# Optimization experiments

Hardware: AMD Instinct MI355X
Metric: run time of the kernel (lower is better)

The kernel has to match this reference:

```python
import jax, jax.numpy as jnp
import numpy as np

EPS = 1e-10

def setup_inputs() -> dict:
    key = jax.random.key(0)
    ks = jax.random.split(key, 7)
    B, S, C, H, W = 8, 4, 512, 64, 64
    Cq = C // 4
    x = jax.random.normal(ks[0], (B, S, C, H, W), dtype=jnp.float32)
    wq = jax.random.normal(ks[1], (S, Cq, C), dtype=jnp.float32) * 0.02
    bq = jax.random.normal(ks[2], (S, Cq), dtype=jnp.float32) * 0.02
    wk = jax.random.normal(ks[3], (S, Cq, C), dtype=jnp.float32) * 0.02
    bk = jax.random.normal(ks[4], (S, Cq), dtype=jnp.float32) * 0.02
    wv = jax.random.normal(ks[5], (S, C, C), dtype=jnp.float32) * 0.02
    bv = jax.random.normal(ks[6], (S, C), dtype=jnp.float32) * 0.02
    gamma = jnp.zeros((1,), dtype=jnp.float32)
    return {"x": x, "wq": wq, "bq": bq, "wk": wk, "bk": bk,
            "wv": wv, "bv": bv, "gamma": gamma}

def reference(x, wq, bq, wk, bk, wv, bv, gamma):
    # x: (B, S, C, H, W); per-scale 1x1 convs == per-pixel matmuls
    B, S, C, H, W = x.shape
    q = jnp.einsum('bschw,soc->bsohw', x, wq) + bq[None, :, :, None, None]
    k = jnp.einsum('bschw,soc->bsohw', x, wk) + bk[None, :, :, None, None]
    v = jnp.einsum('bschw,soc->bsohw', x, wv) + bv[None, :, :, None, None]
    pq = q.reshape(B, S, -1)                      # (B, S, D)
    pk = k.reshape(B, S, -1).transpose(0, 2, 1)   # (B, D, S)
    pv = v.reshape(B, S, -1)                      # (B, S, C*H*W)
    # L2 normalization (cosine similarity), matching torch eps placement
    A1 = pq / (jnp.sqrt(jnp.sum(pq * pq, axis=-1, keepdims=True)) + EPS)
    B1 = pk / (jnp.sqrt(jnp.sum(pk * pk, axis=1, keepdims=True)) + EPS)
    energy = jnp.einsum('bsd,bdt->bst', A1, B1)   # (B, S, S)
    attention = jax.nn.softmax(energy, axis=-1)
    out = jnp.einsum('bst,btd->bsd', attention, pv).reshape(B, S, C, H, W)
    out = gamma[0] * out + x
    # original returns list [out[:, i]] for i in range(S); return stacked tensor
    return out
```

## Files before the change

kernel.cpp:

```cpp
#include <hip/hip_runtime.h>
#include <hip/hip_bf16.h>

#define EPS_F 1e-10f

typedef short s16x8 __attribute__((ext_vector_type(8)));
typedef float f32x4 __attribute__((ext_vector_type(4)));
typedef unsigned short ushort_t;

constexpr int B_ = 8, S_ = 4, C_ = 512, Cq_ = 128, HW_ = 4096;
constexpr long long D_ = (long long)Cq_ * HW_;

__device__ inline float bf_lo(unsigned int u) { return __uint_as_float(u << 16); }
__device__ inline float bf_hi(unsigned int u) { return __uint_as_float(u & 0xffff0000u); }

__device__ inline ushort_t f2bf(float f) {
    __hip_bfloat16 h = __float2bfloat16(f);
    return *reinterpret_cast<ushort_t*>(&h);
}
__device__ inline unsigned int pack_bf2(float a, float b) {
    return (unsigned int)f2bf(a) | ((unsigned int)f2bf(b) << 16);
}
__device__ inline float dot8(uint4 a, uint4 b) {
    return bf_lo(a.x) * bf_lo(b.x) + bf_hi(a.x) * bf_hi(b.x)
         + bf_lo(a.y) * bf_lo(b.y) + bf_hi(a.y) * bf_hi(b.y)
         + bf_lo(a.z) * bf_lo(b.z) + bf_hi(a.z) * bf_hi(b.z)
         + bf_lo(a.w) * bf_lo(b.w) + bf_hi(a.w) * bf_hi(b.w);
}

#define GLOAD16(gp, lp) __builtin_amdgcn_global_load_lds( \
    (const __attribute__((address_space(1))) unsigned int*)(gp), \
    (__attribute__((address_space(3))) unsigned int*)(lp), 16, 0, 0)

#define VMCNT(n) asm volatile("s_waitcnt vmcnt(" #n ")" ::: "memory")
#define LGK0     asm volatile("s_waitcnt lgkmcnt(0)" ::: "memory")
#define MFMA16(a, b, c) __builtin_amdgcn_mfma_f32_16x16x32_bf16(a, b, c, 0, 0, 0)

__global__ __launch_bounds__(256) void prep3(
    const float* __restrict__ wq, const float* __restrict__ wk,
    const float* __restrict__ wv,
    ushort_t* __restrict__ Wqk_pre, ushort_t* __restrict__ Wvb_pre,
    float* __restrict__ g4) {
    int gid = blockIdx.x * 256 + threadIdx.x;
    if (gid < 8 * 24 * 16) g4[gid] = 0.f;
    if (gid < 65536) {
        int s = gid >> 14;
        int kt = (gid >> 11) & 7;
        int row = (gid >> 3) & 255;
        int slot = gid & 7;
        int col = kt * 64 + ((slot ^ (row & 7)) << 3);
        const float* src = (row < 128)
            ? &wq[((size_t)s * 128 + row) * 512 + col]
            : &wk[((size_t)s * 128 + (row - 128)) * 512 + col];
        float4 f0 = *reinterpret_cast<const float4*>(src);
        float4 f1 = *reinterpret_cast<const float4*>(src + 4);
        uint4 o;
        o.x = pack_bf2(f0.x, f0.y); o.y = pack_bf2(f0.z, f0.w);
        o.z = pack_bf2(f1.x, f1.y); o.w = pack_bf2(f1.z, f1.w);
        *reinterpret_cast<uint4*>(Wqk_pre + (size_t)gid * 8) = o;
    } else {
        int c2 = gid - 65536;
        int t = c2 >> 15;
        int ct = (c2 >> 14) & 1;
        int kt = (c2 >> 11) & 7;
        int row = (c2 >> 3) & 255;
        int slot = c2 & 7;
        int col = kt * 64 + ((slot ^ (row & 7)) << 3);
        const float* src = &wv[((size_t)t * 512 + ct * 256 + row) * 512 + col];
        float4 f0 = *reinterpret_cast<const float4*>(src);
        float4 f1 = *reinterpret_cast<const float4*>(src + 4);
        uint4 o;
        o.x = pack_bf2(f0.x, f0.y); o.y = pack_bf2(f0.z, f0.w);
        o.z = pack_bf2(f1.x, f1.y); o.w = pack_bf2(f1.z, f1.w);
        *reinterpret_cast<uint4*>(Wvb_pre + (size_t)c2 * 8) = o;
    }
}

#define STAGE_A(T, bufidx)                                                   \
    { const ushort_t* _tp = ASRC(T);                                         \
      ushort_t* _ld = &AsAll[(bufidx) * 16384];                              \
      _Pragma("unroll")                                                      \
      for (int _i = 0; _i < 4; ++_i)                                         \
          GLOAD16(_tp + ((w4 + _i) << 9) + (lane << 3),                      \
                  _ld + ((w4 + _i) << 9)); }

#define LOAD_B(T, V0, V1)                                                    \
    { const float* _s = BSRC(T);                                             \
      V0 = *reinterpret_cast<const float4*>(_s);                             \
      V1 = *reinterpret_cast<const float4*>(_s + 4); }

#define WRITE_B(bufidx, V0, V1)                                              \
    { float _vv[8] = {V0.x, V0.y, V0.z, V0.w, V1.x, V1.y, V1.z, V1.w};       \
      ushort_t* _bd = &BsAll[(bufidx) * 4096 + bw_row0];                     \
      _Pragma("unroll")                                                      \
      for (int _j = 0; _j < 8; ++_j)                                         \
          _bd[_j * 64 + ((bw_sb ^ _j) << 3)] = f2bf(_vv[_j]); }

#define COMPUTE(bufidx)                                                      \
    { const int _ab = (bufidx) * 16384, _bb = (bufidx) * 4096;               \
      _Pragma("unroll")                                                      \
      for (int h = 0; h < 2; ++h) {                                          \
          s16x8 af0 = *reinterpret_cast<const s16x8*>(                       \
              &AsAll[_ab + (arow + 0 * 16 + li) * 64 + a_sl[h]]);            \
          s16x8 af1 = *reinterpret_cast<const s16x8*>(                       \
              &AsAll[_ab + (arow + 1 * 16 + li) * 64 + a_sl[h]]);            \
          s16x8 af2 = *reinterpret_cast<const s16x8*>(                       \
              &AsAll[_ab + (arow + 2 * 16 + li) * 64 + a_sl[h]]);            \
          s16x8 af3 = *reinterpret_cast<const s16x8*>(                       \
              &AsAll[_ab + (arow + 3 * 16 + li) * 64 + a_sl[h]]);            \
          s16x8 bf0 = *reinterpret_cast<const s16x8*>(                       \
              &BsAll[_bb + bp0 * 64 + b_sl0[h]]);                            \
          s16x8 bf1 = *reinterpret_cast<const s16x8*>(                       \
              &BsAll[_bb + bp1 * 64 + b_sl1[h]]);                            \
          __builtin_amdgcn_s_setprio(1);                                     \
          acc[0][0] = MFMA16(af0, bf0, acc[0][0]);                           \
          acc[0][1] = MFMA16(af0, bf1, acc[0][1]);                           \
          acc[1][0] = MFMA16(af1, bf0, acc[1][0]);                           \
          acc[1][1] = MFMA16(af1, bf1, acc[1][1]);                           \
          acc[2][0] = MFMA16(af2, bf0, acc[2][0]);                           \
          acc[2][1] = MFMA16(af2, bf1, acc[2][1]);                           \
          acc[3][0] = MFMA16(af3, bf0, acc[3][0]);                           \
          acc[3][1] = MFMA16(af3, bf1, acc[3][1]);                           \
          __builtin_amdgcn_s_setprio(0);                                     \
      } }

#define PIPE_PROLOGUE()                                                      \
    LOAD_B(0, nbE0, nbE1);                                                   \
    STAGE_A(0, 0);                                                           \
    LOAD_B(1, nbO0, nbO1);                                                   \
    STAGE_A(1, 1);                                                           \
    VMCNT(10);                                                               \
    WRITE_B(0, nbE0, nbE1);                                                  \
    VMCNT(6);                                                                \
    LGK0;                                                                    \
    __builtin_amdgcn_s_barrier();

#define PIPE_ITER(T, WB0, WB1, LB0, LB1)                                     \
    {                                                                        \
        const int _t = (T);                                                  \
        if (_t + 1 < NT) { VMCNT(4); WRITE_B(oN, WB0, WB1); }                \
        if (_t + 2 < NT) { LOAD_B(_t + 2, LB0, LB1); STAGE_A(_t + 2, oNN); } \
        COMPUTE(oC);                                                         \
        ITER_EXTRA(_t);                                                      \
        if (_t + 1 < NT) {                                                   \
            if (_t + 2 < NT) { VMCNT(6); } else { VMCNT(0); }                \
            LGK0;                                                            \
            __builtin_amdgcn_s_barrier();                                    \
        }                                                                    \
        int _r = oC; oC = oN; oN = oNN; oNN = _r;                            \
    }

#define PIPE_COMMON_DECLS()                                                  \
    const int tid = threadIdx.x;                                             \
    const int w = tid >> 6, lane = tid & 63;                                 \
    const int w4 = w * 4;                                                    \
    const int wr = w >> 1, wc = w & 1;                                       \
    const int li = lane & 15, lk = lane >> 4;                                \
    const int arow = wr * 64;                                                \
    const int bp0 = wc * 32 + li, bp1 = wc * 32 + 16 + li;                   \
    int a_sl[2], b_sl0[2], b_sl1[2];                                         \
    _Pragma("unroll")                                                        \
    for (int h = 0; h < 2; ++h) {                                            \
        a_sl[h] = (((h * 4 + lk) ^ (li & 7)) << 3);                          \
        b_sl0[h] = (((h * 4 + lk) ^ ((bp0 >> 3) & 7) ^ (bp0 & 7)) << 3);     \
        b_sl1[h] = (((h * 4 + lk) ^ ((bp1 >> 3) & 7) ^ (bp1 & 7)) << 3);     \
    }                                                                        \
    const int sk = tid >> 3, sp = (tid & 7) * 8;                             \
    const int bw_row0 = sp * 64 + ((tid >> 3) & 7);                          \
    const int bw_sb = (tid >> 6) ^ (tid & 7);                                \
    int oC = 0, oN = 1, oNN = 2;                                             \
    float4 nbE0, nbE1, nbO0, nbO1;                                           \
    f32x4 acc[4][2];                                                         \
    _Pragma("unroll")                                                        \
    for (int mf = 0; mf < 4; ++mf)                                           \
        _Pragma("unroll")                                                    \
        for (int nf = 0; nf < 2; ++nf) acc[mf][nf] = 0.f;

#define ASRC(T) (Wqk_pre + ((size_t)(s * 8 + (T)) << 14))
#define BSRC(T) (x + (size_t)bt * C_ * HW_ + (size_t)((T) * 64 + sk) * HW_ + p0 + sp)
#define ITER_EXTRA(T)

__global__ __launch_bounds__(512) void qk4(
    const ushort_t* __restrict__ Wqk_pre, const float* __restrict__ x,
    const float* __restrict__ bq, const float* __restrict__ bk,
    ushort_t* __restrict__ Qb, ushort_t* __restrict__ Kb) {

    constexpr int NT = 8;
    const int id = ((blockIdx.x & 7) << 8) | (blockIdx.x >> 3);
    const int bt = id >> 6;
    const int s = bt & 3;
    const int p0 = (id & 63) * 64;

    __shared__ __align__(16) ushort_t AsAll[3 * 16384];
    __shared__ __align__(16) ushort_t BsAll[3 * 4096];

    PIPE_COMMON_DECLS();
    PIPE_PROLOGUE();

    for (int t0 = 0; t0 < NT; t0 += 2) {
        PIPE_ITER(t0,     nbO0, nbO1, nbE0, nbE1);
        PIPE_ITER(t0 + 1, nbE0, nbE1, nbO0, nbO1);
    }

#pragma unroll
    for (int mf = 0; mf < 4; ++mf) {
#pragma unroll
        for (int r = 0; r < 4; ++r) {
            int m = wr * 64 + mf * 16 + lk * 4 + r;
            float bias = (m < 128) ? bq[s * 128 + m] : bk[s * 128 + (m - 128)];
#pragma unroll
            for (int nf = 0; nf < 2; ++nf) {
                int p = p0 + wc * 32 + nf * 16 + li;
                float vv = acc[mf][nf][r] + bias;
                if (m < 128)
                    Qb[(size_t)bt * D_ + (size_t)m * HW_ + p] = f2bf(vv);
                else
                    Kb[(size_t)bt * D_ + (size_t)(m - 128) * HW_ + p] = f2bf(vv);
            }
        }
    }
}
#undef ASRC
#undef BSRC
#undef ITER_EXTRA

#define ASRC(T) (Wvb_pre + (((size_t)(((T) >> 3) * 2 + ct) * 8 + ((T) & 7)) << 14))
#define BSRC(T) (x + ((size_t)(b * 4 + ((T) >> 3)) * 512 + ((T) & 7) * 64 + sk) * HW_ + p0 + sp)
#define ITER_EXTRA(T)                                                        \
    if (((T) & 7) == 7) {                                                    \
        const int _t2 = (T) >> 3;                                            \
        float _wv[4];                                                        \
        _Pragma("unroll")                                                    \
        for (int _so = 0; _so < 4; ++_so) _wv[_so] = attL[_so * 4 + _t2];    \
        _Pragma("unroll")                                                    \
        for (int _so = 0; _so < 4; ++_so)                                    \
            _Pragma("unroll")                                                \
            for (int _mf = 0; _mf < 4; ++_mf)                                \
                _Pragma("unroll")                                            \
                for (int _nf = 0; _nf < 2; ++_nf)                            \
                    mst[_so][_mf][_nf] += _wv[_so] * acc[_mf][_nf];          \
        _Pragma("unroll")                                                    \
        for (int _mf = 0; _mf < 4; ++_mf)                                    \
            _Pragma("unroll")                                                \
            for (int _nf = 0; _nf < 2; ++_nf) acc[_mf][_nf] = 0.f;           \
    }

__global__ __launch_bounds__(512) void vblend4(
    const ushort_t* __restrict__ Wvb_pre, const float* __restrict__ x,
    const float* __restrict__ bv, const float* __restrict__ att,
    const float* __restrict__ gamma, float* __restrict__ out) {

    constexpr int NT = 32;
    const int id = ((blockIdx.x & 7) << 7) | (blockIdx.x >> 3);
    const int b = id >> 7;
    const int ct = (id >> 6) & 1;
    const int p0 = (id & 63) * 64;

    __shared__ __align__(16) ushort_t AsAll[3 * 16384];
    __shared__ __align__(16) ushort_t BsAll[3 * 4096];
    __shared__ float attL[16];

    if (threadIdx.x < 16) attL[threadIdx.x] = att[b * 16 + threadIdx.x];
    __syncthreads();

    PIPE_COMMON_DECLS();

    f32x4 mst[4][4][2];
#pragma unroll
    for (int so = 0; so < 4; ++so)
#pragma unroll
        for (int mf = 0; mf < 4; ++mf)
#pragma unroll
            for (int nf = 0; nf < 2; ++nf) mst[so][mf][nf] = 0.f;

    PIPE_PROLOGUE();

    for (int t0 = 0; t0 < NT; t0 += 2) {
        PIPE_ITER(t0,     nbO0, nbO1, nbE0, nbE1);
        PIPE_ITER(t0 + 1, nbE0, nbE1, nbO0, nbO1);
    }

    const float gm = gamma[0];
    const int c0 = ct * 256;
#pragma unroll
    for (int mf = 0; mf < 4; ++mf) {
#pragma unroll
        for (int r = 0; r < 4; ++r) {
            int c = c0 + wr * 64 + mf * 16 + lk * 4 + r;
            float bvv[4];
#pragma unroll
            for (int t = 0; t < 4; ++t) bvv[t] = bv[(size_t)t * 512 + c];
#pragma unroll
            for (int so = 0; so < 4; ++so) {
                float bsum = attL[so * 4 + 0] * bvv[0] + attL[so * 4 + 1] * bvv[1]
                           + attL[so * 4 + 2] * bvv[2] + attL[so * 4 + 3] * bvv[3];
#pragma unroll
                for (int nf = 0; nf < 2; ++nf) {
                    int p = p0 + wc * 32 + nf * 16 + li;
                    size_t off = ((size_t)(b * 4 + so) * C_ + c) * HW_ + p;
                    out[off] = gm * (mst[so][mf][nf][r] + bsum) + x[off];
                }
            }
        }
    }
}
#undef ASRC
#undef BSRC
#undef ITER_EXTRA

__global__ __launch_bounds__(256) void gram5(
    const ushort_t* __restrict__ Q, const ushort_t* __restrict__ K,
    float* __restrict__ g4) {

    const int ch = blockIdx.x;
    const int b  = blockIdx.y;
    const size_t base = (size_t)ch * (D_ / 16);

    const uint4* qv[4];
    const uint4* kv[4];
#pragma unroll
    for (int s = 0; s < 4; ++s) {
        qv[s] = reinterpret_cast<const uint4*>(Q + (size_t)(b * 4 + s) * D_ + base);
        kv[s] = reinterpret_cast<const uint4*>(K + (size_t)(b * 4 + s) * D_ + base);
    }

    float accr[24];
#pragma unroll
    for (int e = 0; e < 24; ++e) accr[e] = 0.f;

    const int n8 = (int)(D_ / 16 / 8);
    for (int i = threadIdx.x; i < n8; i += 256) {
        uint4 qa[4], ka[4];
#pragma unroll
        for (int s = 0; s < 4; ++s) { qa[s] = qv[s][i]; ka[s] = kv[s][i]; }
#pragma unroll
        for (int s = 0; s < 4; ++s) {
#pragma unroll
            for (int u = 0; u < 4; ++u) accr[s * 4 + u] += dot8(qa[s], ka[u]);
            accr[16 + s] += dot8(qa[s], qa[s]);
            accr[20 + s] += dot8(ka[s], ka[s]);
        }
    }

    __shared__ float red[4][24];
    const int lane = threadIdx.x & 63, wid = threadIdx.x >> 6;
#pragma unroll
    for (int e = 0; e < 24; ++e) {
        float v = accr[e];
#pragma unroll
        for (int o = 32; o > 0; o >>= 1) v += __shfl_down(v, o);
        if (lane == 0) red[wid][e] = v;
    }
    __syncthreads();
    if (threadIdx.x < 24) {
        float t = red[0][threadIdx.x] + red[1][threadIdx.x]
                + red[2][threadIdx.x] + red[3][threadIdx.x];
        g4[((size_t)b * 24 + threadIdx.x) * 16 + ch] = t;
    }
}

__global__ void att_k5(const float* __restrict__ g4, float* __restrict__ att) {
    const int b = threadIdx.x;
    if (b >= B_) return;
    float e_[24];
#pragma unroll
    for (int e = 0; e < 24; ++e) {
        const float* p = g4 + ((size_t)b * 24 + e) * 16;
        float t = 0.f;
#pragma unroll
        for (int ch = 0; ch < 16; ++ch) t += p[ch];
        e_[e] = t;
    }
    float nq[4], nk[4];
#pragma unroll
    for (int s = 0; s < 4; ++s) {
        nq[s] = sqrtf(e_[16 + s]) + EPS_F;
        nk[s] = sqrtf(e_[20 + s]) + EPS_F;
    }
#pragma unroll
    for (int s = 0; s < 4; ++s) {
        float e[4], m = -1e30f;
#pragma unroll
        for (int t = 0; t < 4; ++t) {
            e[t] = e_[s * 4 + t] / (nq[s] * nk[t]);
            m = fmaxf(m, e[t]);
        }
        float sum = 0.f;
#pragma unroll
        for (int t = 0; t < 4; ++t) { e[t] = expf(e[t] - m); sum += e[t]; }
#pragma unroll
        for (int t = 0; t < 4; ++t) att[(size_t)(b * 4 + s) * 4 + t] = e[t] / sum;
    }
}

extern "C" void kernel_launch(void* const* d_in, const int* in_sizes, int n_in,
                              void* d_out, int out_size, void* d_ws, size_t ws_size,
                              hipStream_t stream) {
    const float* x     = (const float*)d_in[0];
    const float* wq    = (const float*)d_in[1];
    const float* bq    = (const float*)d_in[2];
    const float* wk    = (const float*)d_in[3];
    const float* bk    = (const float*)d_in[4];
    const float* wv    = (const float*)d_in[5];
    const float* bv    = (const float*)d_in[6];
    const float* gamma = (const float*)d_in[7];
    float* out = (float*)d_out;

    char* ws = (char*)d_ws;
    const size_t qk_elems = (size_t)B_ * S_ * Cq_ * HW_;
    ushort_t* Qb      = (ushort_t*)ws;
    ushort_t* Kb      = Qb + qk_elems;
    ushort_t* Wqk_pre = Kb + qk_elems;
    ushort_t* Wvb_pre = Wqk_pre + (size_t)4 * 8 * 256 * 64;
    float*    g4      = (float*)(Wvb_pre + (size_t)4 * 2 * 8 * 256 * 64);
    float*    att     = g4 + 8 * 24 * 16;

    prep3<<<768, 256, 0, stream>>>(wq, wk, wv, Wqk_pre, Wvb_pre, g4);
    qk4<<<2048, 512, 0, stream>>>(Wqk_pre, x, bq, bk, Qb, Kb);
    gram5<<<dim3(16, 8), 256, 0, stream>>>(Qb, Kb, g4);
    att_k5<<<1, 64, 0, stream>>>(g4, att);
    vblend4<<<1024, 512, 0, stream>>>(Wvb_pre, x, bv, att, gamma, out);
}
```

Measured before the change: 429.7 us.

## Emit transposed bf16 copy of x in QK kernel and reuse it in V-blend

The QK projection kernel now writes the bf16, swizzled, pixel-major tile of x it already staged in LDS out to a workspace buffer. The V-blend kernel then loads this bf16 tile directly with 16-byte global-to-LDS loads instead of re-reading and converting fp32 x. This halves the bytes x contributes to the V pass and removes the conversion work there. In exchange the QK pass writes an extra 32 MB buffer and needs more workspace; if the workspace is too small it falls back to the old path.

```diff
diff --git a/kernel.cpp b/kernel.cpp
--- a/kernel.cpp
+++ b/kernel.cpp
@@ -219,6 +219,80 @@
         }
     }
 }
+
+__global__ __launch_bounds__(512) void qk5(
+    const ushort_t* __restrict__ Wqk_pre, const float* __restrict__ x,
+    const float* __restrict__ bq, const float* __restrict__ bk,
+    ushort_t* __restrict__ Qb, ushort_t* __restrict__ Kb,
+    ushort_t* __restrict__ xbfT) {
+
+    const int blk = blockIdx.x;
+    const int bt = (blk & 7) * 4 + ((blk >> 3) >> 6);
+    const int s = bt & 3;
+    const int p0 = ((blk >> 3) & 63) * 64;
+
+    __shared__ __align__(16) ushort_t AsAll[3 * 16384];
+    __shared__ __align__(16) ushort_t BsAll[3 * 4096];
+
+    PIPE_COMMON_DECLS();
+
+    const int ep = tid >> 3, esl = tid & 7;
+    const int ec = esl ^ ((ep >> 3) & 7) ^ (ep & 7);
+    ushort_t* emit_base = xbfT + ((size_t)bt * HW_ + p0 + ep) * 512 + ec * 8;
+
+    LOAD_B(0, nbE0, nbE1);
+    STAGE_A(0, 0);
+    LOAD_B(1, nbO0, nbO1);
+    STAGE_A(1, 1);
+    VMCNT(10);
+    WRITE_B(0, nbE0, nbE1);
+    VMCNT(6);
+    LGK0;
+    __builtin_amdgcn_s_barrier();
+
+#pragma unroll
+    for (int t = 0; t < 8; ++t) {
+        if (t + 1 < 8) {
+            if (t == 0) { VMCNT(4); } else { VMCNT(5); }
+            if ((t + 1) & 1) { WRITE_B((t + 1) % 3, nbO0, nbO1); }
+            else             { WRITE_B((t + 1) % 3, nbE0, nbE1); }
+        }
+        if (t + 2 < 8) {
+            if ((t + 2) & 1) { LOAD_B(t + 2, nbO0, nbO1); }
+            else             { LOAD_B(t + 2, nbE0, nbE1); }
+            STAGE_A(t + 2, (t + 2) % 3);
+        }
+        COMPUTE(t % 3);
+        {
+            s16x8 ev = *reinterpret_cast<const s16x8*>(
+                &BsAll[(t % 3) * 4096 + ep * 64 + esl * 8]);
+            *reinterpret_cast<s16x8*>(emit_base + t * 64) = ev;
+        }
+        if (t + 1 < 8) {
+            if (t + 2 < 8) { VMCNT(7); } else { VMCNT(1); }
+            LGK0;
+            __builtin_amdgcn_s_barrier();
+        }
+    }
+
+#pragma unroll
+    for (int mf = 0; mf < 4; ++mf) {
+#pragma unroll
+        for (int r = 0; r < 4; ++r) {
+            int m = wr * 64 + mf * 16 + lk * 4 + r;
+            float bias = (m < 128) ? bq[s * 128 + m] : bk[s * 128 + (m - 128)];
+#pragma unroll
+            for (int nf = 0; nf < 2; ++nf) {
+                int p = p0 + wc * 32 + nf * 16 + li;
+                float vv = acc[mf][nf][r] + bias;
+                if (m < 128)
+                    Qb[(size_t)bt * D_ + (size_t)m * HW_ + p] = f2bf(vv);
+                else
+                    Kb[(size_t)bt * D_ + (size_t)(m - 128) * HW_ + p] = f2bf(vv);
+            }
+        }
+    }
+}
 #undef ASRC
 #undef BSRC
 #undef ITER_EXTRA
@@ -307,6 +381,135 @@
 #undef BSRC
 #undef ITER_EXTRA
 
+__global__ __launch_bounds__(512) void vblend5(
+    const ushort_t* __restrict__ Wvb_pre, const ushort_t* __restrict__ xbfT,
+    const float* __restrict__ x, const float* __restrict__ bv,
+    const float* __restrict__ att, const float* __restrict__ gamma,
+    float* __restrict__ out) {
+
+    const int blk = blockIdx.x;
+    const int b = blk & 7;
+    const int r_ = blk >> 3;
+    const int ct = r_ >> 6;
+    const int p0 = (r_ & 63) * 64;
+
+    __shared__ __align__(16) ushort_t AsAll[3 * 16384];
+    __shared__ __align__(16) ushort_t BsAll[3 * 4096];
+    __shared__ float attL[16];
+
+    if (threadIdx.x < 16) attL[threadIdx.x] = att[b * 16 + threadIdx.x];
+    __syncthreads();
+
+    const int tid = threadIdx.x;
+    const int w = tid >> 6, lane = tid & 63;
+    const int w4 = w * 4;
+    const int wr = w >> 1, wc = w & 1;
+    const int li = lane & 15, lk = lane >> 4;
+    const int arow = wr * 64;
+    const int bp0 = wc * 32 + li, bp1 = wc * 32 + 16 + li;
+    int a_sl[2], b_sl0[2], b_sl1[2];
+#pragma unroll
+    for (int h = 0; h < 2; ++h) {
+        a_sl[h] = (((h * 4 + lk) ^ (li & 7)) << 3);
+        b_sl0[h] = (((h * 4 + lk) ^ ((bp0 >> 3) & 7) ^ (bp0 & 7)) << 3);
+        b_sl1[h] = (((h * 4 + lk) ^ ((bp1 >> 3) & 7) ^ (bp1 & 7)) << 3);
+    }
+    const int sp_ = tid >> 3;
+    const int sc_ = (tid & 7) ^ ((sp_ >> 3) & 7) ^ (sp_ & 7);
+    const ushort_t* bsrc_base = xbfT + ((size_t)b * 4 * HW_) * 512
+                                + ((size_t)(p0 + sp_)) * 512 + sc_ * 8;
+
+    f32x4 acc[4][2];
+#pragma unroll
+    for (int mf = 0; mf < 4; ++mf)
+#pragma unroll
+        for (int nf = 0; nf < 2; ++nf) acc[mf][nf] = 0.f;
+    f32x4 mst[4][4][2];
+#pragma unroll
+    for (int so = 0; so < 4; ++so)
+#pragma unroll
+        for (int mf = 0; mf < 4; ++mf)
+#pragma unroll
+            for (int nf = 0; nf < 2; ++nf) mst[so][mf][nf] = 0.f;
+
+#define STAGE5(T, BUF)                                                       \
+    {   const int _t5 = (T);                                                 \
+        const ushort_t* _ap = Wvb_pre +                                      \
+            (((size_t)((_t5 >> 3) * 2 + ct) * 8 + (_t5 & 7)) << 14);         \
+        ushort_t* _al = &AsAll[(BUF) * 16384];                               \
+        _Pragma("unroll")                                                    \
+        for (int _i = 0; _i < 4; ++_i)                                       \
+            GLOAD16(_ap + ((w4 + _i) << 9) + (lane << 3),                    \
+                    _al + ((w4 + _i) << 9));                                 \
+        const ushort_t* _bp = bsrc_base + (size_t)(_t5 >> 3) * HW_ * 512     \
+                              + (_t5 & 7) * 64;                              \
+        GLOAD16(_bp, &BsAll[(BUF) * 4096 + w * 512]);                        \
+    }
+
+#define BLEND5(TT)                                                           \
+    {   float _w0 = attL[0 * 4 + (TT)], _w1 = attL[1 * 4 + (TT)];            \
+        float _w2 = attL[2 * 4 + (TT)], _w3 = attL[3 * 4 + (TT)];            \
+        _Pragma("unroll")                                                    \
+        for (int _mf = 0; _mf < 4; ++_mf)                                    \
+            _Pragma("unroll")                                                \
+            for (int _nf = 0; _nf < 2; ++_nf) {                              \
+                mst[0][_mf][_nf] += _w0 * acc[_mf][_nf];                     \
+                mst[1][_mf][_nf] += _w1 * acc[_mf][_nf];                     \
+                mst[2][_mf][_nf] += _w2 * acc[_mf][_nf];                     \
+                mst[3][_mf][_nf] += _w3 * acc[_mf][_nf];                     \
+                acc[_mf][_nf] = 0.f;                                         \
+            }                                                                \
+    }
+
+    STAGE5(0, 0);
+    STAGE5(1, 1);
+    VMCNT(5);
+    LGK0;
+    __builtin_amdgcn_s_barrier();
+
+    for (int t = 0; t < 30; ++t) {
+        STAGE5(t + 2, (t + 2) % 3);
+        COMPUTE(t % 3);
+        if ((t & 7) == 7) { BLEND5(t >> 3); }
+        VMCNT(5);
+        LGK0;
+        __builtin_amdgcn_s_barrier();
+    }
+    COMPUTE(0);
+    VMCNT(0);
+    LGK0;
+    __builtin_amdgcn_s_barrier();
+    COMPUTE(1);
+    BLEND5(3);
+
+#undef STAGE5
+#undef BLEND5
+
+    const float gm = gamma[0];
+    const int c0 = ct * 256;
+#pragma unroll
+    for (int mf = 0; mf < 4; ++mf) {
+#pragma unroll
+        for (int r = 0; r < 4; ++r) {
+            int c = c0 + wr * 64 + mf * 16 + lk * 4 + r;
+            float bvv[4];
+#pragma unroll
+            for (int t = 0; t < 4; ++t) bvv[t] = bv[(size_t)t * 512 + c];
+#pragma unroll
+            for (int so = 0; so < 4; ++so) {
+                float bsum = attL[so * 4 + 0] * bvv[0] + attL[so * 4 + 1] * bvv[1]
+                           + attL[so * 4 + 2] * bvv[2] + attL[so * 4 + 3] * bvv[3];
+#pragma unroll
+                for (int nf = 0; nf < 2; ++nf) {
+                    int p = p0 + wc * 32 + nf * 16 + li;
+                    size_t off = ((size_t)(b * 4 + so) * C_ + c) * HW_ + p;
+                    out[off] = gm * (mst[so][mf][nf][r] + bsum) + x[off];
+                }
+            }
+        }
+    }
+}
+
 __global__ __launch_bounds__(256) void gram5(
     const ushort_t* __restrict__ Q, const ushort_t* __restrict__ K,
     float* __restrict__ g4) {
@@ -413,10 +616,22 @@
     ushort_t* Wvb_pre = Wqk_pre + (size_t)4 * 8 * 256 * 64;
     float*    g4      = (float*)(Wvb_pre + (size_t)4 * 2 * 8 * 256 * 64);
     float*    att     = g4 + 8 * 24 * 16;
+    ushort_t* xbfT    = (ushort_t*)(att + 128);
+
+    const size_t need_big =
+        (size_t)((char*)(xbfT + (size_t)32 * HW_ * 512) - ws);
+    const bool big = ws_size >= need_big;
 
     prep3<<<768, 256, 0, stream>>>(wq, wk, wv, Wqk_pre, Wvb_pre, g4);
-    qk4<<<2048, 512, 0, stream>>>(Wqk_pre, x, bq, bk, Qb, Kb);
-    gram5<<<dim3(16, 8), 256, 0, stream>>>(Qb, Kb, g4);
-    att_k5<<<1, 64, 0, stream>>>(g4, att);
-    vblend4<<<1024, 512, 0, stream>>>(Wvb_pre, x, bv, att, gamma, out);
-}
+    if (big) {
+        qk5<<<2048, 512, 0, stream>>>(Wqk_pre, x, bq, bk, Qb, Kb, xbfT);
+        gram5<<<dim3(16, 8), 256, 0, stream>>>(Qb, Kb, g4);
+        att_k5<<<1, 64, 0, stream>>>(g4, att);
+        vblend5<<<1024, 512, 0, stream>>>(Wvb_pre, xbfT, x, bv, att, gamma, out);
+    } else {
+        qk4<<<2048, 512, 0, stream>>>(Wqk_pre, x, bq, bk, Qb, Kb);
+        gram5<<<dim3(16, 8), 256, 0, stream>>>(Qb, Kb, g4);
+        att_k5<<<1, 64, 0, stream>>>(g4, att);
+        vblend4<<<1024, 512, 0, stream>>>(Wvb_pre, x, bv, att, gamma, out);
+    }
+}
```

After: 460.5 us. 1.07x slower.

## Emit transposed bf16 x from QK kernel and reuse it in V-blend GEMM

Applied to the files above, without the earlier changes.

The QK projection kernel now also writes a pixel-major bf16 copy of x into workspace. The V-blend kernel then stages that copy straight into LDS with async global-to-LDS loads, instead of re-reading fp32 x and converting it. Both kernels move from 64-pixel to 32-pixel tiles, drop from triple to double buffering with full vmcnt(0) waits, and declare occupancy 4. This is meant to halve V-side input traffic and raise occupancy. The cost is an extra bf16 write of x, more blocks, and less latency hiding per block.

```diff
diff --git a/kernel.cpp b/kernel.cpp
--- a/kernel.cpp
+++ b/kernel.cpp
@@ -31,9 +31,11 @@
     (const __attribute__((address_space(1))) unsigned int*)(gp), \
     (__attribute__((address_space(3))) unsigned int*)(lp), 16, 0, 0)
 
-#define VMCNT(n) asm volatile("s_waitcnt vmcnt(" #n ")" ::: "memory")
-#define LGK0     asm volatile("s_waitcnt lgkmcnt(0)" ::: "memory")
+#define VMCNT0 asm volatile("s_waitcnt vmcnt(0)" ::: "memory")
+#define LGK0   asm volatile("s_waitcnt lgkmcnt(0)" ::: "memory")
 #define MFMA16(a, b, c) __builtin_amdgcn_mfma_f32_16x16x32_bf16(a, b, c, 0, 0, 0)
+
+#define SWZ(p) ((((p) >> 3) & 7) ^ ((p) & 7))
 
 __global__ __launch_bounds__(256) void prep3(
     const float* __restrict__ wq, const float* __restrict__ wk,
@@ -75,28 +77,79 @@
     }
 }
 
-#define STAGE_A(T, bufidx)                                                   \
-    { const ushort_t* _tp = ASRC(T);                                         \
-      ushort_t* _ld = &AsAll[(bufidx) * 16384];                              \
+
+#define DECLS_COMMON()                                                       \
+    const int tid = threadIdx.x;                                             \
+    const int w = tid >> 6, lane = tid & 63;                                 \
+    const int w4 = w * 4;                                                    \
+    const int wr = w >> 1, wc = w & 1;                                       \
+    const int li = lane & 15, lk = lane >> 4;                                \
+    const int arow = wr * 64;                                                \
+    const int bp = wc * 16 + li;                                             \
+    int a_sl[2], b_sl[2];                                                    \
+    _Pragma("unroll")                                                        \
+    for (int h = 0; h < 2; ++h) {                                            \
+        a_sl[h] = (((h * 4 + lk) ^ (li & 7)) << 3);                          \
+        b_sl[h] = (((h * 4 + lk) ^ SWZ(bp)) << 3);                           \
+    }
+
+__global__ __launch_bounds__(512, 4) void qk6(
+    const ushort_t* __restrict__ Wqk_pre, const float* __restrict__ x,
+    const float* __restrict__ bq, const float* __restrict__ bk,
+    ushort_t* __restrict__ Qb, ushort_t* __restrict__ Kb,
+    ushort_t* __restrict__ xbfT) {
+
+    const int xcd = blockIdx.x & 7;
+    const int idx = blockIdx.x >> 3;
+    const int bt = xcd * 4 + (idx >> 7);
+    const int s = bt & 3;
+    const int p0 = (idx & 127) * 32;
+
+    __shared__ __align__(16) ushort_t AsAll[2 * 16384];
+    __shared__ __align__(16) ushort_t BsAll[2 * 2048];
+
+    DECLS_COMMON();
+
+    const int sk = tid >> 3, spb = (tid & 7) * 4;
+    const int ep = tid >> 3, esl = tid & 7;
+    const int ec = esl ^ SWZ(ep);
+
+    const float* Bx = x + (size_t)bt * C_ * HW_ + p0 + spb;
+
+    f32x4 acc[4];
+#pragma unroll
+    for (int mf = 0; mf < 4; ++mf) acc[mf] = 0.f;
+
+    float4 nb;
+
+#define STAGE_A6(T, BUF)                                                     \
+    { const ushort_t* _tp = Wqk_pre + ((size_t)(s * 8 + (T)) << 14);         \
+      ushort_t* _ld = &AsAll[(BUF) * 16384];                                 \
       _Pragma("unroll")                                                      \
       for (int _i = 0; _i < 4; ++_i)                                         \
           GLOAD16(_tp + ((w4 + _i) << 9) + (lane << 3),                      \
                   _ld + ((w4 + _i) << 9)); }
 
-#define LOAD_B(T, V0, V1)                                                    \
-    { const float* _s = BSRC(T);                                             \
-      V0 = *reinterpret_cast<const float4*>(_s);                             \
-      V1 = *reinterpret_cast<const float4*>(_s + 4); }
-
-#define WRITE_B(bufidx, V0, V1)                                              \
-    { float _vv[8] = {V0.x, V0.y, V0.z, V0.w, V1.x, V1.y, V1.z, V1.w};       \
-      ushort_t* _bd = &BsAll[(bufidx) * 4096 + bw_row0];                     \
-      _Pragma("unroll")                                                      \
-      for (int _j = 0; _j < 8; ++_j)                                         \
-          _bd[_j * 64 + ((bw_sb ^ _j) << 3)] = f2bf(_vv[_j]); }
-
-#define COMPUTE(bufidx)                                                      \
-    { const int _ab = (bufidx) * 16384, _bb = (bufidx) * 4096;               \
+#define LOAD_B6(T) nb = *reinterpret_cast<const float4*>(Bx + (size_t)((T) * 64 + sk) * HW_)
+
+#define WRITE_B6(BUF)                                                        \
+    { float _vv[4] = {nb.x, nb.y, nb.z, nb.w};                               \
+      _Pragma("unroll")                                                      \
+      for (int _j = 0; _j < 4; ++_j) {                                       \
+          int _p = spb + _j;                                                 \
+          BsAll[(BUF) * 2048 + _p * 64 + (((sk >> 3) ^ SWZ(_p)) << 3)        \
+                + (sk & 7)] = f2bf(_vv[_j]);                                 \
+      } }
+
+#define EMIT6(T, BUF)                                                        \
+    if (w < 4) {                                                             \
+        s16x8 _ev = *reinterpret_cast<const s16x8*>(&BsAll[(BUF) * 2048 + tid * 8]); \
+        *reinterpret_cast<s16x8*>(                                           \
+            xbfT + ((size_t)bt * HW_ + p0 + ep) * 512 + (T) * 64 + ec * 8) = _ev; \
+    }
+
+#define COMPUTE6Q(BUF)                                                       \
+    { const int _ab = (BUF) * 16384, _bb = (BUF) * 2048;                     \
       _Pragma("unroll")                                                      \
       for (int h = 0; h < 2; ++h) {                                          \
           s16x8 af0 = *reinterpret_cast<const s16x8*>(                       \
@@ -107,99 +160,39 @@
               &AsAll[_ab + (arow + 2 * 16 + li) * 64 + a_sl[h]]);            \
           s16x8 af3 = *reinterpret_cast<const s16x8*>(                       \
               &AsAll[_ab + (arow + 3 * 16 + li) * 64 + a_sl[h]]);            \
-          s16x8 bf0 = *reinterpret_cast<const s16x8*>(                       \
-              &BsAll[_bb + bp0 * 64 + b_sl0[h]]);                            \
-          s16x8 bf1 = *reinterpret_cast<const s16x8*>(                       \
-              &BsAll[_bb + bp1 * 64 + b_sl1[h]]);                            \
+          s16x8 bf = *reinterpret_cast<const s16x8*>(                        \
+              &BsAll[_bb + bp * 64 + b_sl[h]]);                              \
           __builtin_amdgcn_s_setprio(1);                                     \
-          acc[0][0] = MFMA16(af0, bf0, acc[0][0]);                           \
-          acc[0][1] = MFMA16(af0, bf1, acc[0][1]);                           \
-          acc[1][0] = MFMA16(af1, bf0, acc[1][0]);                           \
-          acc[1][1] = MFMA16(af1, bf1, acc[1][1]);                           \
-          acc[2][0] = MFMA16(af2, bf0, acc[2][0]);                           \
-          acc[2][1] = MFMA16(af2, bf1, acc[2][1]);                           \
-          acc[3][0] = MFMA16(af3, bf0, acc[3][0]);                           \
-          acc[3][1] = MFMA16(af3, bf1, acc[3][1]);                           \
+          acc[0] = MFMA16(af0, bf, acc[0]);                                  \
+          acc[1] = MFMA16(af1, bf, acc[1]);                                  \
+          acc[2] = MFMA16(af2, bf, acc[2]);                                  \
+          acc[3] = MFMA16(af3, bf, acc[3]);                                  \
           __builtin_amdgcn_s_setprio(0);                                     \
       } }
 
-#define PIPE_PROLOGUE()                                                      \
-    LOAD_B(0, nbE0, nbE1);                                                   \
-    STAGE_A(0, 0);                                                           \
-    LOAD_B(1, nbO0, nbO1);                                                   \
-    STAGE_A(1, 1);                                                           \
-    VMCNT(10);                                                               \
-    WRITE_B(0, nbE0, nbE1);                                                  \
-    VMCNT(6);                                                                \
-    LGK0;                                                                    \
+    LOAD_B6(0);
+    STAGE_A6(0, 0);
+    WRITE_B6(0);
+    VMCNT0; LGK0;
     __builtin_amdgcn_s_barrier();
 
-#define PIPE_ITER(T, WB0, WB1, LB0, LB1)                                     \
-    {                                                                        \
-        const int _t = (T);                                                  \
-        if (_t + 1 < NT) { VMCNT(4); WRITE_B(oN, WB0, WB1); }                \
-        if (_t + 2 < NT) { LOAD_B(_t + 2, LB0, LB1); STAGE_A(_t + 2, oNN); } \
-        COMPUTE(oC);                                                         \
-        ITER_EXTRA(_t);                                                      \
-        if (_t + 1 < NT) {                                                   \
-            if (_t + 2 < NT) { VMCNT(6); } else { VMCNT(0); }                \
-            LGK0;                                                            \
-            __builtin_amdgcn_s_barrier();                                    \
-        }                                                                    \
-        int _r = oC; oC = oN; oN = oNN; oNN = _r;                            \
-    }
-
-#define PIPE_COMMON_DECLS()                                                  \
-    const int tid = threadIdx.x;                                             \
-    const int w = tid >> 6, lane = tid & 63;                                 \
-    const int w4 = w * 4;                                                    \
-    const int wr = w >> 1, wc = w & 1;                                       \
-    const int li = lane & 15, lk = lane >> 4;                                \
-    const int arow = wr * 64;                                                \
-    const int bp0 = wc * 32 + li, bp1 = wc * 32 + 16 + li;                   \
-    int a_sl[2], b_sl0[2], b_sl1[2];                                         \
-    _Pragma("unroll")                                                        \
-    for (int h = 0; h < 2; ++h) {                                            \
-        a_sl[h] = (((h * 4 + lk) ^ (li & 7)) << 3);                          \
-        b_sl0[h] = (((h * 4 + lk) ^ ((bp0 >> 3) & 7) ^ (bp0 & 7)) << 3);     \
-        b_sl1[h] = (((h * 4 + lk) ^ ((bp1 >> 3) & 7) ^ (bp1 & 7)) << 3);     \
-    }                                                                        \
-    const int sk = tid >> 3, sp = (tid & 7) * 8;                             \
-    const int bw_row0 = sp * 64 + ((tid >> 3) & 7);                          \
-    const int bw_sb = (tid >> 6) ^ (tid & 7);                                \
-    int oC = 0, oN = 1, oNN = 2;                                             \
-    float4 nbE0, nbE1, nbO0, nbO1;                                           \
-    f32x4 acc[4][2];                                                         \
-    _Pragma("unroll")                                                        \
-    for (int mf = 0; mf < 4; ++mf)                                           \
-        _Pragma("unroll")                                                    \
-        for (int nf = 0; nf < 2; ++nf) acc[mf][nf] = 0.f;
-
-#define ASRC(T) (Wqk_pre + ((size_t)(s * 8 + (T)) << 14))
-#define BSRC(T) (x + (size_t)bt * C_ * HW_ + (size_t)((T) * 64 + sk) * HW_ + p0 + sp)
-#define ITER_EXTRA(T)
-
-__global__ __launch_bounds__(512) void qk4(
-    const ushort_t* __restrict__ Wqk_pre, const float* __restrict__ x,
-    const float* __restrict__ bq, const float* __restrict__ bk,
-    ushort_t* __restrict__ Qb, ushort_t* __restrict__ Kb) {
-
-    constexpr int NT = 8;
-    const int id = ((blockIdx.x & 7) << 8) | (blockIdx.x >> 3);
-    const int bt = id >> 6;
-    const int s = bt & 3;
-    const int p0 = (id & 63) * 64;
-
-    __shared__ __align__(16) ushort_t AsAll[3 * 16384];
-    __shared__ __align__(16) ushort_t BsAll[3 * 4096];
-
-    PIPE_COMMON_DECLS();
-    PIPE_PROLOGUE();
-
-    for (int t0 = 0; t0 < NT; t0 += 2) {
-        PIPE_ITER(t0,     nbO0, nbO1, nbE0, nbE1);
-        PIPE_ITER(t0 + 1, nbE0, nbE1, nbO0, nbO1);
-    }
+#pragma unroll
+    for (int t = 0; t < 8; ++t) {
+        if (t < 7) { LOAD_B6(t + 1); STAGE_A6(t + 1, (t + 1) & 1); }
+        EMIT6(t, t & 1);
+        COMPUTE6Q(t & 1);
+        if (t < 7) {
+            WRITE_B6((t + 1) & 1);
+            VMCNT0; LGK0;
+            __builtin_amdgcn_s_barrier();
+        }
+    }
+
+#undef STAGE_A6
+#undef LOAD_B6
+#undef WRITE_B6
+#undef EMIT6
+#undef COMPUTE6Q
 
 #pragma unroll
     for (int mf = 0; mf < 4; ++mf) {
@@ -207,77 +200,115 @@
         for (int r = 0; r < 4; ++r) {
             int m = wr * 64 + mf * 16 + lk * 4 + r;
             float bias = (m < 128) ? bq[s * 128 + m] : bk[s * 128 + (m - 128)];
-#pragma unroll
-            for (int nf = 0; nf < 2; ++nf) {
-                int p = p0 + wc * 32 + nf * 16 + li;
-                float vv = acc[mf][nf][r] + bias;
-                if (m < 128)
-                    Qb[(size_t)bt * D_ + (size_t)m * HW_ + p] = f2bf(vv);
-                else
-                    Kb[(size_t)bt * D_ + (size_t)(m - 128) * HW_ + p] = f2bf(vv);
-            }
-        }
-    }
-}
-#undef ASRC
-#undef BSRC
-#undef ITER_EXTRA
-
-#define ASRC(T) (Wvb_pre + (((size_t)(((T) >> 3) * 2 + ct) * 8 + ((T) & 7)) << 14))
-#define BSRC(T) (x + ((size_t)(b * 4 + ((T) >> 3)) * 512 + ((T) & 7) * 64 + sk) * HW_ + p0 + sp)
-#define ITER_EXTRA(T)                                                        \
-    if (((T) & 7) == 7) {                                                    \
-        const int _t2 = (T) >> 3;                                            \
-        float _wv[4];                                                        \
-        _Pragma("unroll")                                                    \
-        for (int _so = 0; _so < 4; ++_so) _wv[_so] = attL[_so * 4 + _t2];    \
-        _Pragma("unroll")                                                    \
-        for (int _so = 0; _so < 4; ++_so)                                    \
-            _Pragma("unroll")                                                \
-            for (int _mf = 0; _mf < 4; ++_mf)                                \
-                _Pragma("unroll")                                            \
-                for (int _nf = 0; _nf < 2; ++_nf)                            \
-                    mst[_so][_mf][_nf] += _wv[_so] * acc[_mf][_nf];          \
-        _Pragma("unroll")                                                    \
-        for (int _mf = 0; _mf < 4; ++_mf)                                    \
-            _Pragma("unroll")                                                \
-            for (int _nf = 0; _nf < 2; ++_nf) acc[_mf][_nf] = 0.f;           \
-    }
-
-__global__ __launch_bounds__(512) void vblend4(
-    const ushort_t* __restrict__ Wvb_pre, const float* __restrict__ x,
-    const float* __restrict__ bv, const float* __restrict__ att,
-    const float* __restrict__ gamma, float* __restrict__ out) {
-
-    constexpr int NT = 32;
-    const int id = ((blockIdx.x & 7) << 7) | (blockIdx.x >> 3);
-    const int b = id >> 7;
-    const int ct = (id >> 6) & 1;
-    const int p0 = (id & 63) * 64;
-
-    __shared__ __align__(16) ushort_t AsAll[3 * 16384];
-    __shared__ __align__(16) ushort_t BsAll[3 * 4096];
-    __shared__ float attL[16];
-
-    if (threadIdx.x < 16) attL[threadIdx.x] = att[b * 16 + threadIdx.x];
-    __syncthreads();
-
-    PIPE_COMMON_DECLS();
-
-    f32x4 mst[4][4][2];
+            int p = p0 + wc * 16 + li;
+            float vv = acc[mf][r] + bias;
+            if (m < 128)
+                Qb[(size_t)bt * D_ + (size_t)m * HW_ + p] = f2bf(vv);
+            else
+                Kb[(size_t)bt * D_ + (size_t)(m - 128) * HW_ + p] = f2bf(vv);
+        }
+    }
+}
+
+__global__ __launch_bounds__(512, 4) void vblend6(
+    const ushort_t* __restrict__ Wvb_pre, const ushort_t* __restrict__ xbfT,
+    const float* __restrict__ x, const float* __restrict__ bv,
+    const float* __restrict__ att, const float* __restrict__ gamma,
+    float* __restrict__ out) {
+
+    const int b = blockIdx.x & 7;
+    const int r_ = blockIdx.x >> 3;
+    const int ct = r_ >> 7;
+    const int p0 = (r_ & 127) * 32;
+
+    __shared__ __align__(16) ushort_t AsAll[2 * 16384];
+    __shared__ __align__(16) ushort_t BsAll[2 * 2048];
+
+    DECLS_COMMON();
+
+    float attv[16];
+#pragma unroll
+    for (int i = 0; i < 16; ++i)
+        attv[i] = __uint_as_float(__builtin_amdgcn_readfirstlane(
+            __float_as_uint(att[b * 16 + i])));
+
+    const int sp_ = tid >> 3;
+    const int sc_ = (tid & 7) ^ SWZ(sp_);
+    const ushort_t* bsrc = xbfT + ((size_t)b * 4 * HW_ + p0 + sp_) * 512 + sc_ * 8;
+
+    f32x4 acc[4];
+    f32x4 mst[4][4];
+#pragma unroll
+    for (int mf = 0; mf < 4; ++mf) acc[mf] = 0.f;
 #pragma unroll
     for (int so = 0; so < 4; ++so)
 #pragma unroll
-        for (int mf = 0; mf < 4; ++mf)
-#pragma unroll
-            for (int nf = 0; nf < 2; ++nf) mst[so][mf][nf] = 0.f;
-
-    PIPE_PROLOGUE();
-
-    for (int t0 = 0; t0 < NT; t0 += 2) {
-        PIPE_ITER(t0,     nbO0, nbO1, nbE0, nbE1);
-        PIPE_ITER(t0 + 1, nbE0, nbE1, nbO0, nbO1);
-    }
+        for (int mf = 0; mf < 4; ++mf) mst[so][mf] = 0.f;
+
+#define STAGE6(T, BUF)                                                       \
+    { const ushort_t* _ap = Wvb_pre +                                        \
+          (((size_t)(((T) >> 3) * 2 + ct) * 8 + ((T) & 7)) << 14);           \
+      ushort_t* _al = &AsAll[(BUF) * 16384];                                 \
+      _Pragma("unroll")                                                      \
+      for (int _i = 0; _i < 4; ++_i)                                         \
+          GLOAD16(_ap + ((w4 + _i) << 9) + (lane << 3),                      \
+                  _al + ((w4 + _i) << 9));                                   \
+      if (w < 4)                                                             \
+          GLOAD16(bsrc + (size_t)((T) >> 3) * HW_ * 512 + ((T) & 7) * 64,    \
+                  &BsAll[(BUF) * 2048 + w * 512]); }
+
+#define COMPUTE6(BUF)                                                        \
+    { const int _ab = (BUF) * 16384, _bb = (BUF) * 2048;                     \
+      _Pragma("unroll")                                                      \
+      for (int h = 0; h < 2; ++h) {                                          \
+          s16x8 af0 = *reinterpret_cast<const s16x8*>(                       \
+              &AsAll[_ab + (arow + 0 * 16 + li) * 64 + a_sl[h]]);            \
+          s16x8 af1 = *reinterpret_cast<const s16x8*>(                       \
+              &AsAll[_ab + (arow + 1 * 16 + li) * 64 + a_sl[h]]);            \
+          s16x8 af2 = *reinterpret_cast<const s16x8*>(                       \
+              &AsAll[_ab + (arow + 2 * 16 + li) * 64 + a_sl[h]]);            \
+          s16x8 af3 = *reinterpret_cast<const s16x8*>(                       \
+              &AsAll[_ab + (arow + 3 * 16 + li) * 64 + a_sl[h]]);            \
+          s16x8 bf = *reinterpret_cast<const s16x8*>(                        \
+              &BsAll[_bb + bp * 64 + b_sl[h]]);                              \
+          __builtin_amdgcn_s_setprio(1);                                     \
+          acc[0] = MFMA16(af0, bf, acc[0]);                                  \
+          acc[1] = MFMA16(af1, bf, acc[1]);                                  \
+          acc[2] = MFMA16(af2, bf, acc[2]);                                  \
+          acc[3] = MFMA16(af3, bf, acc[3]);                                  \
+          __builtin_amdgcn_s_setprio(0);                                     \
+      } }
+
+#define BLEND6(T2)                                                           \
+    { _Pragma("unroll")                                                      \
+      for (int _so = 0; _so < 4; ++_so)                                      \
+          _Pragma("unroll")                                                  \
+          for (int _mf = 0; _mf < 4; ++_mf)                                  \
+              mst[_so][_mf] += attv[_so * 4 + (T2)] * acc[_mf];              \
+      _Pragma("unroll")                                                      \
+      for (int _mf = 0; _mf < 4; ++_mf) acc[_mf] = 0.f; }
+
+    STAGE6(0, 0);
+    VMCNT0;
+    __builtin_amdgcn_s_barrier();
+
+#pragma unroll
+    for (int t = 0; t < 32; ++t) {
+        if (t < 31) STAGE6(t + 1, (t + 1) & 1);
+        COMPUTE6(t & 1);
+        if (t == 7)  BLEND6(0);
+        if (t == 15) BLEND6(1);
+        if (t == 23) BLEND6(2);
+        if (t == 31) BLEND6(3);
+        if (t < 31) {
+            VMCNT0; LGK0;
+            __builtin_amdgcn_s_barrier();
+        }
+    }
+
+#undef STAGE6
+#undef COMPUTE6
+#undef BLEND6
 
     const float gm = gamma[0];
     const int c0 = ct * 256;
@@ -291,21 +322,15 @@
             for (int t = 0; t < 4; ++t) bvv[t] = bv[(size_t)t * 512 + c];
 #pragma unroll
             for (int so = 0; so < 4; ++so) {
-                float bsum = attL[so * 4 + 0] * bvv[0] + attL[so * 4 + 1] * bvv[1]
-                           + attL[so * 4 + 2] * bvv[2] + attL[so * 4 + 3] * bvv[3];
-#pragma unroll
-                for (int nf = 0; nf < 2; ++nf) {
-                    int p = p0 + wc * 32 + nf * 16 + li;
-                    size_t off = ((size_t)(b * 4 + so) * C_ + c) * HW_ + p;
-                    out[off] = gm * (mst[so][mf][nf][r] + bsum) + x[off];
-                }
+                float bsum = attv[so * 4 + 0] * bvv[0] + attv[so * 4 + 1] * bvv[1]
+                           + attv[so * 4 + 2] * bvv[2] + attv[so * 4 + 3] * bvv[3];
+                int p = p0 + wc * 16 + li;
+                size_t off = ((size_t)(b * 4 + so) * C_ + c) * HW_ + p;
+                out[off] = gm * (mst[so][mf][r] + bsum) + x[off];
             }
         }
     }
 }
-#undef ASRC
-#undef BSRC
-#undef ITER_EXTRA
 
 __global__ __launch_bounds__(256) void gram5(
     const ushort_t* __restrict__ Q, const ushort_t* __restrict__ K,
@@ -413,10 +438,11 @@
     ushort_t* Wvb_pre = Wqk_pre + (size_t)4 * 8 * 256 * 64;
     float*    g4      = (float*)(Wvb_pre + (size_t)4 * 2 * 8 * 256 * 64);
     float*    att     = g4 + 8 * 24 * 16;
+    ushort_t* xbfT    = (ushort_t*)(att + 128);
 
     prep3<<<768, 256, 0, stream>>>(wq, wk, wv, Wqk_pre, Wvb_pre, g4);
-    qk4<<<2048, 512, 0, stream>>>(Wqk_pre, x, bq, bk, Qb, Kb);
+    qk6<<<4096, 512, 0, stream>>>(Wqk_pre, x, bq, bk, Qb, Kb, xbfT);
     gram5<<<dim3(16, 8), 256, 0, stream>>>(Qb, Kb, g4);
     att_k5<<<1, 64, 0, stream>>>(g4, att);
-    vblend4<<<1024, 512, 0, stream>>>(Wvb_pre, x, bv, att, gamma, out);
-}
+    vblend6<<<2048, 512, 0, stream>>>(Wvb_pre, xbfT, x, bv, att, gamma, out);
+}
```

New measurement: 507.5 us. +18.1%, slower.
